# Optimization experiments

Hardware: AMD Instinct MI355X
Metric: run time of the kernel (lower is better)

The kernel has to match this reference:

```python
import jax, jax.numpy as jnp
import numpy as np

NUM_VECTORS = 8192
LATENT_DIM = 256
BETA = 0.25
B, H, W = 16, 32, 32


def setup_inputs() -> dict:
    key = jax.random.key(0)
    k1, k2, k3 = jax.random.split(key, 3)
    x = jax.random.normal(k1, (B, LATENT_DIM, H, W), dtype=jnp.float32)
    # embedding_key.weight.data.uniform_(-1/num_vectors, 1/num_vectors)
    emb_key = jax.random.uniform(
        k2, (NUM_VECTORS, LATENT_DIM), dtype=jnp.float32,
        minval=-1.0 / NUM_VECTORS, maxval=1.0 / NUM_VECTORS)
    # orthogonal init for embedding_value
    a = np.asarray(jax.random.normal(k3, (LATENT_DIM, LATENT_DIM), dtype=jnp.float32))
    q, r = np.linalg.qr(a)
    q = q * np.sign(np.diag(r))  # make deterministic-ish orthogonal
    emb_value = jnp.asarray(q, dtype=jnp.float32)
    return {"x": x, "emb_key": emb_key, "emb_value": emb_value}


def reference(x, emb_key, emb_value):
    b, c, h, w = x.shape
    xt = jnp.transpose(x, (0, 2, 3, 1))          # b h w c
    xf = xt.reshape(-1, c)                       # (bhw) c
    d = (jnp.sum(xf * xf, axis=1, keepdims=True)
         + jnp.sum(emb_key * emb_key, axis=1)
         - 2.0 * (xf @ emb_key.T))               # (bhw) K
    idx = jnp.argmin(d, axis=1)                  # (bhw,)
    xq = emb_key[idx] @ emb_value                # (bhw) c
    xq = xq.reshape(xt.shape)                    # b h w c
    xq_grad = jnp.transpose(xq, (0, 3, 1, 2))    # b c h w
    sg = jax.lax.stop_gradient
    loss = jnp.mean((sg(xq) - xt) ** 2) + BETA * jnp.mean((xq - sg(xt)) ** 2)
    xq_st = xt + sg(xq - xt)                     # straight-through
    xq_st = jnp.transpose(xq_st, (0, 3, 1, 2))   # b c h w
    return xq_st, xq_grad, idx, loss
```

## Files before the change

### kernel.cpp

```cpp
#include <hip/hip_runtime.h>
#include <cfloat>

#define LATENT 256
#define NV 8192
#define NROWS 16384
#define HW 1024
#define CHW (LATENT * HW)
#define PLANE 4194304
#define IDX_OFF (2 * PLANE)
#define LOSS_OFF (IDX_OFF + NROWS)
#define MARGIN_S 6e-4f
#define CAP 2048

typedef __bf16 bf16x8 __attribute__((ext_vector_type(8)));
typedef float f32x4 __attribute__((ext_vector_type(4)));

__device__ inline unsigned short f2bf(float f) {
  unsigned u = __builtin_bit_cast(unsigned, f);
  u = u + 0x7FFFu + ((u >> 16) & 1u);
  return (unsigned short)(u >> 16);
}
__device__ inline float bf2f(unsigned short h) {
  return __builtin_bit_cast(float, (unsigned)h << 16);
}

__global__ __launch_bounds__(256) void prep_ek(const float* __restrict__ ek,
                                               unsigned short* __restrict__ ek_hi) {
  int i = (blockIdx.x * 256 + threadIdx.x) << 3;
  float4 a = *(const float4*)(ek + i);
  float4 b = *(const float4*)(ek + i + 4);
  ushort4 h0, h1;
  h0.x = f2bf(a.x); h0.y = f2bf(a.y); h0.z = f2bf(a.z); h0.w = f2bf(a.w);
  h1.x = f2bf(b.x); h1.y = f2bf(b.y); h1.z = f2bf(b.z); h1.w = f2bf(b.w);
  *(ushort4*)(ek_hi + i) = h0;
  *(ushort4*)(ek_hi + i + 4) = h1;
}

__global__ __launch_bounds__(256) void prep_x(const float* __restrict__ x,
                                              unsigned short* __restrict__ x_hi) {
  __shared__ float tile[64][68];
  const int t = threadIdx.x;
  const int b = blockIdx.x >> 6;
  const int c0 = ((blockIdx.x >> 4) & 3) << 6;
  const int hw0 = (blockIdx.x & 15) << 6;
  #pragma unroll
  for (int p = 0; p < 4; ++p) {
    int id = (p << 8) + t;
    int r = id >> 4;
    int h4 = (id & 15) << 2;
    float4 v = *(const float4*)(x + (size_t)b * CHW + (size_t)(c0 + r) * HW + hw0 + h4);
    *(float4*)&tile[r][h4] = v;
  }
  __syncthreads();
  #pragma unroll
  for (int p = 0; p < 4; ++p) {
    int id = (p << 8) + t;
    int rh = id >> 4;
    int c4 = (id & 15) << 2;
    ushort4 h;
    h.x = f2bf(tile[c4][rh]);     h.y = f2bf(tile[c4 + 1][rh]);
    h.z = f2bf(tile[c4 + 2][rh]); h.w = f2bf(tile[c4 + 3][rh]);
    *(ushort4*)(x_hi + (size_t)((b << 10) + hw0 + rh) * LATENT + c0 + c4) = h;
  }
}

__global__ __launch_bounds__(256, 4) void phaseA(const unsigned short* __restrict__ ek_hi,
                                                 const unsigned short* __restrict__ x_hi,
                                                 unsigned* __restrict__ smax) {
  __shared__ unsigned short As[2][4][128][8];
  __shared__ unsigned short Bs[2][4][128][8];
  const int t = threadIdx.x;
  const int mt = blockIdx.x & 63;
  const int panel = blockIdx.x >> 6;
  const int m0 = mt << 7, r0 = panel << 7;
  const int sside = t >> 7;
  const int sr = t & 127;
  const unsigned short* src = sside ? x_hi + (size_t)(r0 + sr) * LATENT
                                    : ek_hi + (size_t)(m0 + sr) * LATENT;
  uint4 reg[4];
  #pragma unroll
  for (int q = 0; q < 4; ++q) reg[q] = *(const uint4*)(src + (q << 3));
  {
    unsigned short (*dst)[128][8] = sside ? Bs[0] : As[0];
    #pragma unroll
    for (int q = 0; q < 4; ++q) *(uint4*)&dst[q][sr][0] = reg[q];
  }
  const int w = t >> 6, l = t & 63;
  const int lm = l & 15, q4 = l >> 4;
  const int mw = (w & 1) << 6;
  const int nw = (w >> 1) << 6;
  f32x4 acc[4][4];
  #pragma unroll
  for (int ms = 0; ms < 4; ++ms)
    #pragma unroll
    for (int ns = 0; ns < 4; ++ns) acc[ms][ns] = (f32x4){0.f, 0.f, 0.f, 0.f};
  for (int kc = 0; kc < 8; ++kc) {
    const int buf = kc & 1;
    __syncthreads();
    if (kc < 7) {
      #pragma unroll
      for (int q = 0; q < 4; ++q)
        reg[q] = *(const uint4*)(src + ((kc + 1) << 5) + (q << 3));
    }
    bf16x8 a[4], b[4];
    #pragma unroll
    for (int ms = 0; ms < 4; ++ms)
      a[ms] = *(const bf16x8*)&As[buf][q4][mw + (ms << 4) + lm][0];
    #pragma unroll
    for (int ns = 0; ns < 4; ++ns)
      b[ns] = *(const bf16x8*)&Bs[buf][q4][nw + (ns << 4) + lm][0];
    #pragma unroll
    for (int ms = 0; ms < 4; ++ms)
      #pragma unroll
      for (int ns = 0; ns < 4; ++ns)
        acc[ms][ns] = __builtin_amdgcn_mfma_f32_16x16x32_bf16(a[ms], b[ns], acc[ms][ns], 0, 0, 0);
    if (kc < 7) {
      unsigned short (*dst)[128][8] = sside ? Bs[buf ^ 1] : As[buf ^ 1];
      #pragma unroll
      for (int q = 0; q < 4; ++q) *(uint4*)&dst[q][sr][0] = reg[q];
    }
  }
  unsigned* stg = (unsigned*)&As[0][0][0][0];
  const int lbase = (l >> 4) << 2;
  #pragma unroll
  for (int ms = 0; ms < 4; ++ms) {
    #pragma unroll
    for (int ns = 0; ns < 4; ++ns) {
      f32x4 v4 = acc[ms][ns];
      float mx = fmaxf(fmaxf(v4[0], v4[1]), fmaxf(v4[2], v4[3]));
      mx = fmaxf(mx, __shfl_xor(mx, 16, 64));
      mx = fmaxf(mx, __shfl_xor(mx, 32, 64));
      float th = mx - MARGIN_S;
      unsigned mk = 0;
      #pragma unroll
      for (int r = 0; r < 4; ++r) if (v4[r] >= th) mk |= 1u << (lbase + r);
      mk |= (unsigned)__shfl_xor((int)mk, 16, 64);
      mk |= (unsigned)__shfl_xor((int)mk, 32, 64);
      if (l < 16) {
        int sloc = ((w & 1) << 2) + ms;
        int rloc = nw + (ns << 4) + l;
        stg[(sloc << 7) + rloc] = (unsigned)f2bf(mx) | (mk << 16);
      }
    }
  }
  __syncthreads();
  #pragma unroll
  for (int p = 0; p < 4; ++p) {
    int wid = (p << 8) + t;
    int sloc = wid >> 7;
    int rloc = wid & 127;
    smax[(size_t)((mt << 3) + sloc) * NROWS + r0 + rloc] = stg[wid];
  }
}

__global__ __launch_bounds__(256) void phaseB(const float* __restrict__ x,
                                              const float* __restrict__ ek,
                                              const unsigned* __restrict__ smax,
                                              int* __restrict__ idxw,
                                              float* __restrict__ out) {
  __shared__ float xs[64][257];
  __shared__ float pmax[64][4];
  __shared__ float thrs[64];
  __shared__ float Xs[64];
  __shared__ unsigned long long best[64];
  __shared__ unsigned list[CAP];
  __shared__ int cnt;
  const int t = threadIdx.x;
  const int row0 = blockIdx.x << 6;
  const int b = row0 >> 10;
  const int hw0 = row0 & 1023;
  if (t == 0) cnt = 0;
  if (t < 64) best[t] = ~0ull;
  #pragma unroll
  for (int p = 0; p < 16; ++p) {
    int id = (p << 8) + t;
    int c = id >> 4;
    int r4 = (id & 15) << 2;
    float4 v = *(const float4*)(x + (size_t)b * CHW + (size_t)c * HW + hw0 + r4);
    xs[r4 + 0][c] = v.x; xs[r4 + 1][c] = v.y; xs[r4 + 2][c] = v.z; xs[r4 + 3][c] = v.w;
  }
  {
    const int r = t >> 2, q = t & 3;
    float m = -FLT_MAX;
    #pragma unroll 8
    for (int i = 0; i < 128; ++i) {
      unsigned wd = smax[(size_t)((i << 2) + q) * NROWS + row0 + r];
      m = fmaxf(m, bf2f((unsigned short)(wd & 0xffffu)));
    }
    pmax[r][q] = m;
  }
  __syncthreads();
  if (t < 64) {
    thrs[t] = fmaxf(fmaxf(pmax[t][0], pmax[t][1]), fmaxf(pmax[t][2], pmax[t][3])) - MARGIN_S;
    double s = 0.0;
    for (int c = 0; c < 256; ++c) {
      double v = (double)xs[t][c];
      s = fma(v, v, s);
    }
    Xs[t] = (float)s;
  }
  __syncthreads();
  {
    const int r = t >> 2, q = t & 3;
    const float thr = thrs[r];
    for (int i = 0; i < 128; ++i) {
      unsigned wd = smax[(size_t)((i << 2) + q) * NROWS + row0 + r];
      if (bf2f((unsigned short)(wd & 0xffffu)) >= thr) {
        unsigned mk = wd >> 16;
        int sidx = (i << 2) + q;
        while (mk) {
          int bit = __builtin_ctz(mk);
          mk &= mk - 1;
          int k = (sidx << 4) + bit;
          int slot = atomicAdd(&cnt, 1);
          if (slot < CAP) {
            list[slot] = ((unsigned)r << 13) | (unsigned)k;
          } else {
            const float* xr = &xs[r][0];
            const float* ep = ek + (size_t)k * LATENT;
            float f = 0.f;
            #pragma unroll 8
            for (int c = 0; c < 256; ++c) f = fmaf(xr[c], ep[c], f);
            float d = fmaf(-2.f, f, Xs[r]);
            unsigned u = __builtin_bit_cast(unsigned, d);
            u ^= (u >> 31) ? 0xFFFFFFFFu : 0x80000000u;
            atomicMin(&best[r], ((unsigned long long)u << 32) | (unsigned)k);
          }
        }
      }
    }
  }
  __syncthreads();
  const int n = cnt < CAP ? cnt : CAP;
  for (int i = t; i < n; i += 256) {
    unsigned enc = list[i];
    int r = enc >> 13;
    int k = enc & 0x1fff;
    const float* xr = &xs[r][0];
    const float* ep = ek + (size_t)k * LATENT;
    float f = 0.f;
    #pragma unroll 8
    for (int c = 0; c < 256; ++c) f = fmaf(xr[c], ep[c], f);
    float d = fmaf(-2.f, f, Xs[r]);
    unsigned u = __builtin_bit_cast(unsigned, d);
    u ^= (u >> 31) ? 0xFFFFFFFFu : 0x80000000u;
    atomicMin(&best[r], ((unsigned long long)u << 32) | (unsigned)k);
  }
  __syncthreads();
  if (t < 64) {
    int k = (int)(best[t] & 0xFFFFFFFFu);
    idxw[row0 + t] = k;
    out[IDX_OFF + row0 + t] = (float)k;
  }
}

__global__ __launch_bounds__(256) void out_kernel(
    const float* __restrict__ ek, const float* __restrict__ ev,
    const float* __restrict__ x, const int* __restrict__ idxw,
    float* __restrict__ out, float* __restrict__ bsum) {
  __shared__ float As[32][68];
  __shared__ float Vs[32][260];
  __shared__ int idx_s[64];
  __shared__ float red[256];
  const int t = threadIdx.x;
  const int blk = blockIdx.x;
  const int i0 = blk << 6;
  if (t < 64) idx_s[t] = idxw[i0 + t];
  const int ty = t >> 5;
  const int tx = t & 31;
  float acc[8][8];
  #pragma unroll
  for (int r = 0; r < 8; ++r)
    #pragma unroll
    for (int j = 0; j < 8; ++j) acc[r][j] = 0.f;
  for (int cc = 0; cc < 8; ++cc) {
    __syncthreads();
    {
      int r = t >> 2, cl = (t & 3) << 3;
      const float* eb = ek + (size_t)idx_s[r] * LATENT + (cc << 5) + cl;
      float4 v0 = *(const float4*)eb;
      float4 v1 = *(const float4*)(eb + 4);
      As[cl + 0][r] = v0.x; As[cl + 1][r] = v0.y;
      As[cl + 2][r] = v0.z; As[cl + 3][r] = v0.w;
      As[cl + 4][r] = v1.x; As[cl + 5][r] = v1.y;
      As[cl + 6][r] = v1.z; As[cl + 7][r] = v1.w;
    }
    {
      int c = t >> 3, jb = (t & 7) << 5;
      const float* vb = ev + (size_t)((cc << 5) + c) * LATENT + jb;
      float4* dst = (float4*)&Vs[c][jb];
      #pragma unroll
      for (int q = 0; q < 8; ++q) dst[q] = *(const float4*)(vb + 4 * q);
    }
    __syncthreads();
    #pragma unroll
    for (int c = 0; c < 32; ++c) {
      float a[8], bv[8];
      *(float4*)&a[0] = *(const float4*)&As[c][ty << 3];
      *(float4*)&a[4] = *(const float4*)&As[c][(ty << 3) + 4];
      *(float4*)&bv[0] = *(const float4*)&Vs[c][tx << 3];
      *(float4*)&bv[4] = *(const float4*)&Vs[c][(tx << 3) + 4];
      #pragma unroll
      for (int r = 0; r < 8; ++r)
        #pragma unroll
        for (int j = 0; j < 8; ++j) acc[r][j] = fmaf(a[r], bv[j], acc[r][j]);
    }
  }
  const int bb = i0 >> 10;
  const int rbase = (i0 & 1023) + (ty << 3);
  float lsum = 0.f;
  #pragma unroll
  for (int j = 0; j < 8; ++j) {
    int jc = (tx << 3) + j;
    const float* xp = x + (size_t)bb * CHW + (size_t)jc * HW + rbase;
    float* o0 = out + (size_t)bb * CHW + (size_t)jc * HW + rbase;
    float* o1 = o0 + PLANE;
    float st[8], xq0[8];
    #pragma unroll
    for (int r = 0; r < 8; ++r) {
      float xq = acc[r][j];
      float xt = xp[r];
      float tmp = xq - xt;
      lsum = fmaf(tmp, tmp, lsum);
      st[r] = xt + tmp;
      xq0[r] = xq;
    }
    *(float4*)(o0 + 0) = make_float4(st[0], st[1], st[2], st[3]);
    *(float4*)(o0 + 4) = make_float4(st[4], st[5], st[6], st[7]);
    *(float4*)(o1 + 0) = make_float4(xq0[0], xq0[1], xq0[2], xq0[3]);
    *(float4*)(o1 + 4) = make_float4(xq0[4], xq0[5], xq0[6], xq0[7]);
  }
  red[t] = lsum;
  __syncthreads();
  for (int s = 128; s > 0; s >>= 1) {
    if (t < s) red[t] += red[t + s];
    __syncthreads();
  }
  if (t == 0) bsum[blk] = red[0];
}

__global__ __launch_bounds__(256) void fin_kernel(const float* __restrict__ bsum,
                                                  float* __restrict__ out) {
  __shared__ float red[256];
  int t = threadIdx.x;
  red[t] = bsum[t];
  __syncthreads();
  for (int s = 128; s > 0; s >>= 1) {
    if (t < s) red[t] += red[t + s];
    __syncthreads();
  }
  if (t == 0) {
    float m = red[0] / (float)PLANE;
    out[LOSS_OFF] = m + 0.25f * m;
  }
}

extern "C" void kernel_launch(void* const* d_in, const int* in_sizes, int n_in,
                              void* d_out, int out_size, void* d_ws, size_t ws_size,
                              hipStream_t stream) {
  const float* x = (const float*)d_in[0];
  const float* ek = (const float*)d_in[1];
  const float* ev = (const float*)d_in[2];
  float* out = (float*)d_out;
  char* base = (char*)d_ws;
  unsigned short* ek_hi = (unsigned short*)(base);
  unsigned short* x_hi  = (unsigned short*)(base + 4194304);
  int*            idxw  = (int*)(base + 12582912);
  float*          bsum  = (float*)(base + 12648448);
  unsigned* smax = (unsigned*)d_out;

  prep_ek<<<1024, 256, 0, stream>>>(ek, ek_hi);
  prep_x<<<1024, 256, 0, stream>>>(x, x_hi);
  phaseA<<<8192, 256, 0, stream>>>(ek_hi, x_hi, smax);
  phaseB<<<256, 256, 0, stream>>>(x, ek, smax, idxw, out);
  out_kernel<<<256, 256, 0, stream>>>(ek, ev, x, idxw, out, bsum);
  fin_kernel<<<1, 256, 0, stream>>>(bsum, out);
}
```

Before: 273.0 us.

## Use direct global-to-LDS loads in phaseA and stage epilogue stores through LDS

phaseA now fills its shared tiles with global_load_lds instructions instead of loading into registers and then writing LDS. This drops the register staging and frees VGPRs, but the async loads now have to complete in time for the barrier. The final output kernel also stages x reads and output writes through shared memory, so each thread does contiguous coalesced float4 global accesses instead of strided per-thread patterns. The cost is several extra barriers per channel iteration in the epilogue.

```diff
diff --git a/kernel.cpp b/kernel.cpp
--- a/kernel.cpp
+++ b/kernel.cpp
@@ -15,6 +15,10 @@
 typedef __bf16 bf16x8 __attribute__((ext_vector_type(8)));
 typedef float f32x4 __attribute__((ext_vector_type(4)));
 
+typedef __attribute__((address_space(1))) const unsigned int GU32;
+typedef __attribute__((address_space(3))) unsigned int SU32;
+#define GLOAD16(gp, sp) __builtin_amdgcn_global_load_lds((GU32*)(gp), (SU32*)(sp), 16, 0, 0)
+
 __device__ inline unsigned short f2bf(float f) {
   unsigned u = __builtin_bit_cast(unsigned, f);
   u = u + 0x7FFFu + ((u >> 16) & 1u);
@@ -73,18 +77,19 @@
   const int mt = blockIdx.x & 63;
   const int panel = blockIdx.x >> 6;
   const int m0 = mt << 7, r0 = panel << 7;
+  const int sr = t & 127;
   const int sside = t >> 7;
-  const int sr = t & 127;
   const unsigned short* src = sside ? x_hi + (size_t)(r0 + sr) * LATENT
                                     : ek_hi + (size_t)(m0 + sr) * LATENT;
-  uint4 reg[4];
-  #pragma unroll
-  for (int q = 0; q < 4; ++q) reg[q] = *(const uint4*)(src + (q << 3));
-  {
-    unsigned short (*dst)[128][8] = sside ? Bs[0] : As[0];
-    #pragma unroll
-    for (int q = 0; q < 4; ++q) *(uint4*)&dst[q][sr][0] = reg[q];
-  }
+  const int row0 = ((t >> 6) & 1) << 6;
+  unsigned short (*SD)[4][128][8] = sside ? Bs : As;
+#define STAGEA(buf, kc) { \
+    const unsigned short* g_ = src + ((kc) << 5); \
+    GLOAD16(g_,      &SD[buf][0][row0][0]); \
+    GLOAD16(g_ + 8,  &SD[buf][1][row0][0]); \
+    GLOAD16(g_ + 16, &SD[buf][2][row0][0]); \
+    GLOAD16(g_ + 24, &SD[buf][3][row0][0]); }
+  STAGEA(0, 0);
   const int w = t >> 6, l = t & 63;
   const int lm = l & 15, q4 = l >> 4;
   const int mw = (w & 1) << 6;
@@ -97,11 +102,7 @@
   for (int kc = 0; kc < 8; ++kc) {
     const int buf = kc & 1;
     __syncthreads();
-    if (kc < 7) {
-      #pragma unroll
-      for (int q = 0; q < 4; ++q)
-        reg[q] = *(const uint4*)(src + ((kc + 1) << 5) + (q << 3));
-    }
+    if (kc < 7) STAGEA(buf ^ 1, kc + 1);
     bf16x8 a[4], b[4];
     #pragma unroll
     for (int ms = 0; ms < 4; ++ms)
@@ -114,11 +115,6 @@
       #pragma unroll
       for (int ns = 0; ns < 4; ++ns)
         acc[ms][ns] = __builtin_amdgcn_mfma_f32_16x16x32_bf16(a[ms], b[ns], acc[ms][ns], 0, 0, 0);
-    if (kc < 7) {
-      unsigned short (*dst)[128][8] = sside ? Bs[buf ^ 1] : As[buf ^ 1];
-      #pragma unroll
-      for (int q = 0; q < 4; ++q) *(uint4*)&dst[q][sr][0] = reg[q];
-    }
   }
   unsigned* stg = (unsigned*)&As[0][0][0][0];
   const int lbase = (l >> 4) << 2;
@@ -151,6 +147,7 @@
     int rloc = wid & 127;
     smax[(size_t)((mt << 3) + sloc) * NROWS + r0 + rloc] = stg[wid];
   }
+#undef STAGEA
 }
 
 __global__ __launch_bounds__(256) void phaseB(const float* __restrict__ x,
@@ -306,29 +303,43 @@
         for (int j = 0; j < 8; ++j) acc[r][j] = fmaf(a[r], bv[j], acc[r][j]);
     }
   }
+  __syncthreads();
   const int bb = i0 >> 10;
-  const int rbase = (i0 & 1023) + (ty << 3);
+  const int hwb = i0 & 1023;
+  float* xL  = &As[0][0];
+  float* stL = &Vs[0][0];
+  float* xqL = stL + 32 * 68;
+  const int ch = t >> 3;
+  const int part = t & 7;
   float lsum = 0.f;
-  #pragma unroll
   for (int j = 0; j < 8; ++j) {
-    int jc = (tx << 3) + j;
-    const float* xp = x + (size_t)bb * CHW + (size_t)jc * HW + rbase;
-    float* o0 = out + (size_t)bb * CHW + (size_t)jc * HW + rbase;
-    float* o1 = o0 + PLANE;
-    float st[8], xq0[8];
-    #pragma unroll
-    for (int r = 0; r < 8; ++r) {
-      float xq = acc[r][j];
-      float xt = xp[r];
-      float tmp = xq - xt;
-      lsum = fmaf(tmp, tmp, lsum);
-      st[r] = xt + tmp;
-      xq0[r] = xq;
-    }
-    *(float4*)(o0 + 0) = make_float4(st[0], st[1], st[2], st[3]);
-    *(float4*)(o0 + 4) = make_float4(st[4], st[5], st[6], st[7]);
-    *(float4*)(o1 + 0) = make_float4(xq0[0], xq0[1], xq0[2], xq0[3]);
-    *(float4*)(o1 + 4) = make_float4(xq0[4], xq0[5], xq0[6], xq0[7]);
+    {
+      const float* xp = x + (size_t)bb * CHW + (size_t)((ch << 3) + j) * HW + hwb + (part << 3);
+      *(float4*)&xL[ch * 68 + (part << 3)] = *(const float4*)xp;
+      *(float4*)&xL[ch * 68 + (part << 3) + 4] = *(const float4*)(xp + 4);
+    }
+    __syncthreads();
+    {
+      #pragma unroll
+      for (int r = 0; r < 8; ++r) {
+        float xq = acc[r][j];
+        float xt = xL[tx * 68 + (ty << 3) + r];
+        float tmp = xq - xt;
+        lsum = fmaf(tmp, tmp, lsum);
+        stL[tx * 68 + (ty << 3) + r] = xt + tmp;
+        xqL[tx * 68 + (ty << 3) + r] = xq;
+      }
+    }
+    __syncthreads();
+    {
+      float* o0 = out + (size_t)bb * CHW + (size_t)((ch << 3) + j) * HW + hwb + (part << 3);
+      float* o1 = o0 + PLANE;
+      *(float4*)o0       = *(const float4*)&stL[ch * 68 + (part << 3)];
+      *(float4*)(o0 + 4) = *(const float4*)&stL[ch * 68 + (part << 3) + 4];
+      *(float4*)o1       = *(const float4*)&xqL[ch * 68 + (part << 3)];
+      *(float4*)(o1 + 4) = *(const float4*)&xqL[ch * 68 + (part << 3) + 4];
+    }
+    __syncthreads();
   }
   red[t] = lsum;
   __syncthreads();
```

Result: slower. 302.6 us (+10.9%).
